# Performance work log

Hardware: AMD Instinct MI355X
Metric: run time of the kernel (lower is better)

The kernel has to match this reference:

```python
import jax, jax.numpy as jnp
import numpy as np

N_LAYERS = 2
D_MODEL = 1024
D_INNER = 2 * D_MODEL
D_STATE = 16
D_CONV = 4
DT_RANK = D_MODEL // 16  # 64
B_SZ, L = 1, 2048
EPS = 1e-5


def layernorm(x, w, b):
    mu = jnp.mean(x, axis=-1, keepdims=True)
    var = jnp.mean(jnp.square(x - mu), axis=-1, keepdims=True)
    return (x - mu) * jax.lax.rsqrt(var + EPS) * w + b


def mamba(x, in_w, cw, cb, xp_w, dtp_w, dtp_b, A_log, Dp, out_w):
    # x: [B, L, D_MODEL]
    Bn, Ln, _ = x.shape
    xz = jnp.einsum('bld,ed->ble', x, in_w)          # [B,L,2*D_INNER]
    xc, z = jnp.split(xz, 2, axis=-1)
    # causal depthwise conv1d (kernel D_CONV)
    xp = jnp.pad(xc, ((0, 0), (D_CONV - 1, 0), (0, 0)))
    xc = sum(xp[:, k:k + Ln, :] * cw[:, k] for k in range(D_CONV)) + cb
    xc = jax.nn.silu(xc)
    dbl = jnp.einsum('ble,re->blr', xc, xp_w)        # [B,L,DT_RANK+2*D_STATE]
    dt, Bm, Cm = jnp.split(dbl, [DT_RANK, DT_RANK + D_STATE], axis=-1)
    dt = jax.nn.softplus(jnp.einsum('blr,er->ble', dt, dtp_w) + dtp_b)  # [B,L,E]
    A = -jnp.exp(A_log)                              # [E,N], strictly negative
    dA = jnp.exp(dt[..., None] * A)                  # [B,L,E,N]
    dBu = (dt * xc)[..., None] * Bm[:, :, None, :]   # [B,L,E,N]

    def step(h, inp):
        dA_t, dBu_t, C_t = inp
        h = dA_t * h + dBu_t                         # [B,E,N]
        y = jnp.einsum('ben,bn->be', h, C_t)
        return h, y

    h0 = jnp.zeros((Bn, D_INNER, D_STATE), dA.dtype)
    _, ys = jax.lax.scan(step, h0, (dA.transpose(1, 0, 2, 3),
                                    dBu.transpose(1, 0, 2, 3),
                                    Cm.transpose(1, 0, 2)))
    y = ys.transpose(1, 0, 2) + xc * Dp              # [B,L,E]
    y = y * jax.nn.silu(z)
    return jnp.einsum('ble,de->bld', y, out_w)       # [B,L,D_MODEL]


def setup_inputs() -> dict:
    key = jax.random.key(0)
    ks = jax.random.split(key, 12)
    s = 0.02
    dt_init = np.log(np.expm1(0.01)).astype(np.float32)  # softplus^-1(0.01)
    A_row = jnp.log(jnp.arange(1, D_STATE + 1, dtype=jnp.float32))
    return {
        'x': jax.random.normal(ks[0], (B_SZ, L, D_MODEL), jnp.float32),
        'ln_w': jnp.ones((N_LAYERS, D_MODEL), jnp.float32),
        'ln_b': jnp.zeros((N_LAYERS, D_MODEL), jnp.float32),
        'in_proj_w': jax.random.normal(ks[1], (N_LAYERS, 2 * D_INNER, D_MODEL)) * s,
        'conv_w': jax.random.normal(ks[2], (N_LAYERS, D_INNER, D_CONV)) * 0.2,
        'conv_b': jnp.zeros((N_LAYERS, D_INNER), jnp.float32),
        'x_proj_w': jax.random.normal(ks[3], (N_LAYERS, DT_RANK + 2 * D_STATE, D_INNER)) * s,
        'dt_proj_w': jax.random.normal(ks[4], (N_LAYERS, D_INNER, DT_RANK)) * (DT_RANK ** -0.5),
        'dt_proj_b': jnp.full((N_LAYERS, D_INNER), dt_init),
        'A_log': jnp.broadcast_to(A_row, (N_LAYERS, D_INNER, D_STATE)).copy(),
        'D_skip': jnp.ones((N_LAYERS, D_INNER), jnp.float32),
        'out_proj_w': jax.random.normal(ks[5], (N_LAYERS, D_MODEL, D_INNER)) * s,
        'norm_f_w': jnp.ones((D_MODEL,), jnp.float32),
        'norm_f_b': jnp.zeros((D_MODEL,), jnp.float32),
    }


def reference(x, ln_w, ln_b, in_proj_w, conv_w, conv_b, x_proj_w, dt_proj_w,
              dt_proj_b, A_log, D_skip, out_proj_w, norm_f_w, norm_f_b):
    for i in range(N_LAYERS):
        h = layernorm(x, ln_w[i], ln_b[i])
        h = mamba(h, in_proj_w[i], conv_w[i], conv_b[i], x_proj_w[i],
                  dt_proj_w[i], dt_proj_b[i], A_log[i], D_skip[i], out_proj_w[i])
        x = h + x  # residual (dropout/drop_path are identity in eval)
    return layernorm(x, norm_f_w, norm_f_b)
```

## Files before the change

kernel.cpp:

```cpp
#include <hip/hip_runtime.h>
#include <hip/hip_bf16.h>
#include <math.h>

#define LSEQ 2048
#define DMODEL 1024
#define DINNER 2048
#define DSTATE 16
#define DCONV 4
#define DTRANK 64
#define RPROJ 96

#define CHUNK 16
#define NCHUNK (LSEQ / CHUNK)

#define XSPLIT 4

typedef __attribute__((ext_vector_type(8))) short bf16x8;
typedef __attribute__((ext_vector_type(4))) float f32x4;

__device__ __forceinline__ float softplusf(float x) {
    return (x > 20.f) ? x : log1pf(__expf(x));
}
__device__ __forceinline__ float siluf(float x) {
    return x / (1.f + __expf(-x));
}
__device__ __forceinline__ short f2bf(float f) {
    union { float f; unsigned u; } v; v.f = f;
    unsigned r = v.u + 0x7FFFu + ((v.u >> 16) & 1u);
    return (short)(r >> 16);
}
__device__ __forceinline__ float bf2f(short h) {
    union { unsigned u; float f; } v;
    v.u = ((unsigned)(unsigned short)h) << 16;
    return v.f;
}

__device__ __forceinline__ void cvt8(const float* __restrict__ s,
                                     short* __restrict__ d, int i) {
    const float4 a = *(const float4*)(s + i);
    const float4 b = *(const float4*)(s + i + 4);
    alignas(16) short h[8];
    h[0] = f2bf(a.x); h[1] = f2bf(a.y); h[2] = f2bf(a.z); h[3] = f2bf(a.w);
    h[4] = f2bf(b.x); h[5] = f2bf(b.y); h[6] = f2bf(b.z); h[7] = f2bf(b.w);
    *(uint4*)(d + i) = *(const uint4*)h;
}

__global__ __launch_bounds__(256) void cvt_weights(
    const float* __restrict__ s0, short* __restrict__ d0, int n0,
    const float* __restrict__ s1, short* __restrict__ d1, int n1,
    const float* __restrict__ s2, short* __restrict__ d2, int n2,
    const float* __restrict__ s3, short* __restrict__ d3, int n3)
{
    int i = (blockIdx.x * 256 + threadIdx.x) * 8;
    if (i < n0) { cvt8(s0, d0, i); return; }
    i -= n0;
    if (i < n1) { cvt8(s1, d1, i); return; }
    i -= n1;
    if (i < n2) { cvt8(s2, d2, i); return; }
    i -= n2;
    if (i < n3) { cvt8(s3, d3, i); return; }
}

__global__ __launch_bounds__(256) void ln_kernel(
    const float* __restrict__ x, const float* __restrict__ w,
    const float* __restrict__ b, float* __restrict__ outf,
    short* __restrict__ outb)
{
    __shared__ float s1[256], s2[256];
    const int row = blockIdx.x;
    const int tid = threadIdx.x;
    const float* xr = x + (size_t)row * DMODEL;
    float v[4];
    float s = 0.f, sq = 0.f;
#pragma unroll
    for (int k = 0; k < 4; k++) {
        v[k] = xr[k * 256 + tid];
        s += v[k];
        sq += v[k] * v[k];
    }
    s1[tid] = s; s2[tid] = sq;
    __syncthreads();
    for (int off = 128; off > 0; off >>= 1) {
        if (tid < off) { s1[tid] += s1[tid + off]; s2[tid] += s2[tid + off]; }
        __syncthreads();
    }
    const float mu = s1[0] * (1.f / DMODEL);
    const float var = s2[0] * (1.f / DMODEL) - mu * mu;
    const float rstd = rsqrtf(var + 1e-5f);
#pragma unroll
    for (int k = 0; k < 4; k++) {
        const int i = k * 256 + tid;
        const float o = (v[k] - mu) * rstd * w[i] + b[i];
        if (outf) outf[(size_t)row * DMODEL + i] = o;
        if (outb) outb[(size_t)row * DMODEL + i] = f2bf(o);
    }
}

template<int NJ, int MODE>
__global__ __launch_bounds__(256) void gemm_mfma(
    const short* __restrict__ A, int lda,
    const short* __restrict__ W, int ldw,
    float* __restrict__ Cf, short* __restrict__ Cb, int ldc,
    int M, int N, int K,
    const float* __restrict__ bias,
    const float* __restrict__ resid,
    size_t csplit)
{
    constexpr int BN = 32 * NJ;
    constexpr int HN = 16 * NJ;
    constexpr int WISS = BN / 64;
    __shared__ alignas(16) short As[64 * 32];
    __shared__ alignas(16) short Ws[BN * 32];

    const int tid = threadIdx.x;
    const int lane = tid & 63;
    const int w = tid >> 6;
    const int wr = w >> 1, wc = w & 1;
    const int row0 = blockIdx.y * 64;
    const int col0 = blockIdx.x * BN;
    const int kbeg = blockIdx.z * K;

    const int srow = tid >> 2;
    const int skch = ((tid & 3) ^ ((srow >> 1) & 3)) * 8;

    f32x4 acc[2][NJ];
#pragma unroll
    for (int i = 0; i < 2; i++)
#pragma unroll
        for (int j = 0; j < NJ; j++) acc[i][j] = (f32x4)0.f;

    const int lrow = lane & 15;
    const int q = lane >> 4;

    for (int kt = kbeg; kt < kbeg + K; kt += 32) {
        __syncthreads();
        {
            const short* gp = A + (size_t)(row0 + srow) * lda + kt + skch;
            __builtin_amdgcn_global_load_lds(
                (const __attribute__((address_space(1))) void*)gp,
                (__attribute__((address_space(3))) void*)(As + tid * 8), 16, 0, 0);
        }
#pragma unroll
        for (int j = 0; j < WISS; j++) {
            const int wrow = col0 + j * 64 + srow;
            if (wrow < N) {
                const short* gp = W + (size_t)wrow * ldw + kt + skch;
                __builtin_amdgcn_global_load_lds(
                    (const __attribute__((address_space(1))) void*)gp,
                    (__attribute__((address_space(3))) void*)(Ws + j * 2048 + tid * 8),
                    16, 0, 0);
            }
        }
        __syncthreads();

        bf16x8 af[2], bfr[NJ];
#pragma unroll
        for (int i = 0; i < 2; i++) {
            const int R = wr * 32 + i * 16 + lrow;
            af[i] = *(const bf16x8*)&As[R * 32 + ((q ^ ((R >> 1) & 3)) * 8)];
        }
#pragma unroll
        for (int j = 0; j < NJ; j++) {
            const int R = wc * HN + j * 16 + lrow;
            bfr[j] = *(const bf16x8*)&Ws[R * 32 + ((q ^ ((R >> 1) & 3)) * 8)];
        }
#pragma unroll
        for (int i = 0; i < 2; i++)
#pragma unroll
            for (int j = 0; j < NJ; j++)
                acc[i][j] = __builtin_amdgcn_mfma_f32_16x16x32_bf16(
                    af[i], bfr[j], acc[i][j], 0, 0, 0);
    }

    if (MODE == 0 && csplit) Cf += blockIdx.z * csplit;

    const int rbase = row0 + wr * 32;
    const int cbase = col0 + wc * HN;
#pragma unroll
    for (int i = 0; i < 2; i++) {
#pragma unroll
        for (int j = 0; j < NJ; j++) {
            const int gcol = cbase + j * 16 + lrow;
            if (gcol < N) {
#pragma unroll
                for (int r = 0; r < 4; r++) {
                    const int grow = rbase + i * 16 + (lane >> 4) * 4 + r;
                    float v = acc[i][j][r];
                    if (MODE == 2) v += resid[(size_t)grow * ldc + gcol];
                    if (MODE == 5) v = softplusf(v + bias[gcol]);
                    if (MODE == 3 || MODE == 5) {
                        Cb[(size_t)grow * ldc + gcol] = f2bf(v);
                    } else {
                        Cf[(size_t)grow * ldc + gcol] = v;
                    }
                }
            }
        }
    }
}

__global__ __launch_bounds__(256) void combine_xproj(
    const float* __restrict__ part,
    float* __restrict__ dbl, short* __restrict__ dblb)
{
    const int i = (blockIdx.x * 256 + threadIdx.x) * 4;
    const int S = LSEQ * RPROJ;
    float4 v = *(const float4*)(part + i);
#pragma unroll
    for (int s = 1; s < XSPLIT; s++) {
        const float4 p = *(const float4*)(part + s * S + i);
        v.x += p.x; v.y += p.y; v.z += p.z; v.w += p.w;
    }
    *(float4*)(dbl + i) = v;
    alignas(8) short h[4] = {f2bf(v.x), f2bf(v.y), f2bf(v.z), f2bf(v.w)};
    *(unsigned long long*)(dblb + i) = *(const unsigned long long*)h;
}

__global__ __launch_bounds__(256) void conv_silu_kernel(
    const short* __restrict__ xzb, const float* __restrict__ cw,
    const float* __restrict__ cb, short* __restrict__ xcb)
{
    const int g = blockIdx.x * 256 + threadIdx.x;
    const int t = g >> 8;
    const int c0 = (g & 255) * 8;
    float acc[8];
#pragma unroll
    for (int j = 0; j < 8; j++) acc[j] = cb[c0 + j];
#pragma unroll
    for (int k = 0; k < DCONV; k++) {
        const int tt = t - (DCONV - 1) + k;
        if (tt >= 0) {
            const bf16x8 v = *(const bf16x8*)(xzb + (size_t)tt * (2 * DINNER) + c0);
#pragma unroll
            for (int j = 0; j < 8; j++)
                acc[j] += bf2f(v[j]) * cw[(c0 + j) * DCONV + k];
        }
    }
    alignas(16) short h[8];
#pragma unroll
    for (int j = 0; j < 8; j++) h[j] = f2bf(siluf(acc[j]));
    *(uint4*)(xcb + (size_t)t * DINNER + c0) = *(const uint4*)h;
}

__global__ __launch_bounds__(256) void scan_pass1(
    const short* __restrict__ dtb,
    const short* __restrict__ xcb,
    const float* __restrict__ dbl,
    const float* __restrict__ A_log,
    float* __restrict__ S,
    float* __restrict__ sumdt)
{
    const int e = blockIdx.x * 256 + threadIdx.x;
    const int c = blockIdx.y;
    float a[DSTATE];
#pragma unroll
    for (int n = 0; n < DSTATE; n++) a[n] = -__expf(A_log[(size_t)e * DSTATE + n]);
    float h[DSTATE];
#pragma unroll
    for (int n = 0; n < DSTATE; n++) h[n] = 0.f;
    float sd = 0.f;

    __shared__ float sBC[CHUNK][32];
    for (int i = threadIdx.x; i < CHUNK * 32; i += 256) {
        const int tl = i >> 5, j = i & 31;
        sBC[tl][j] = dbl[(size_t)(c * CHUNK + tl) * RPROJ + DTRANK + j];
    }
    __syncthreads();

    const size_t rb = (size_t)c * CHUNK * DINNER + e;
    short dt_c = dtb[rb], xc_c = xcb[rb];
#pragma unroll
    for (int tl = 0; tl < CHUNK; tl++) {
        short dt_n = 0, xc_n = 0;
        if (tl + 1 < CHUNK) {
            dt_n = dtb[rb + (size_t)(tl + 1) * DINNER];
            xc_n = xcb[rb + (size_t)(tl + 1) * DINNER];
        }
        const float dtv = bf2f(dt_c);
        const float du = dtv * bf2f(xc_c);
        sd += dtv;
#pragma unroll
        for (int n = 0; n < DSTATE; n++) {
            const float dA = __expf(dtv * a[n]);
            h[n] = dA * h[n] + du * sBC[tl][n];
        }
        dt_c = dt_n; xc_c = xc_n;
    }
    sumdt[(size_t)c * DINNER + e] = sd;
#pragma unroll
    for (int n = 0; n < DSTATE; n++)
        S[((size_t)c * DSTATE + n) * DINNER + e] = h[n];
}

__global__ __launch_bounds__(256) void scan_pass2(
    const float* __restrict__ A_log,
    const float* __restrict__ sumdt,
    float* __restrict__ S)
{
    const int idx = blockIdx.x * 256 + threadIdx.x;
    const int e = idx & (DINNER - 1);
    const int n = idx >> 11;
    const float a = -__expf(A_log[(size_t)e * DSTATE + n]);
    float H = 0.f;
    for (int c = 0; c < NCHUNK; c++) {
        const size_t off = ((size_t)c * DSTATE + n) * DINNER + e;
        const float tmp = S[off];
        S[off] = H;
        const float P = __expf(a * sumdt[(size_t)c * DINNER + e]);
        H = P * H + tmp;
    }
}

__global__ __launch_bounds__(256) void scan_pass3(
    const short* __restrict__ dtb,
    const short* __restrict__ xcb,
    const float* __restrict__ dbl,
    const short* __restrict__ xzb,
    const float* __restrict__ A_log,
    const float* __restrict__ Dp,
    const float* __restrict__ S,
    short* __restrict__ yb)
{
    const int e = blockIdx.x * 256 + threadIdx.x;
    const int c = blockIdx.y;
    float a[DSTATE];
#pragma unroll
    for (int n = 0; n < DSTATE; n++) a[n] = -__expf(A_log[(size_t)e * DSTATE + n]);
    float h[DSTATE];
#pragma unroll
    for (int n = 0; n < DSTATE; n++)
        h[n] = S[((size_t)c * DSTATE + n) * DINNER + e];
    const float dskip = Dp[e];

    __shared__ float sBC[CHUNK][32];
    for (int i = threadIdx.x; i < CHUNK * 32; i += 256) {
        const int tl = i >> 5, j = i & 31;
        sBC[tl][j] = dbl[(size_t)(c * CHUNK + tl) * RPROJ + DTRANK + j];
    }
    __syncthreads();

    const size_t rb = (size_t)c * CHUNK * DINNER + e;
    const size_t zb = (size_t)c * CHUNK * (2 * DINNER) + DINNER + e;
    short dt_c = dtb[rb], xc_c = xcb[rb], z_c = xzb[zb];
#pragma unroll
    for (int tl = 0; tl < CHUNK; tl++) {
        short dt_n = 0, xc_n = 0, z_n = 0;
        if (tl + 1 < CHUNK) {
            dt_n = dtb[rb + (size_t)(tl + 1) * DINNER];
            xc_n = xcb[rb + (size_t)(tl + 1) * DINNER];
            z_n = xzb[zb + (size_t)(tl + 1) * (2 * DINNER)];
        }
        const float dtv = bf2f(dt_c);
        const float xcv = bf2f(xc_c);
        const float du = dtv * xcv;
        float yv = 0.f;
#pragma unroll
        for (int n = 0; n < DSTATE; n++) {
            const float dA = __expf(dtv * a[n]);
            h[n] = dA * h[n] + du * sBC[tl][n];
            yv += h[n] * sBC[tl][16 + n];
        }
        yv = (yv + xcv * dskip) * siluf(bf2f(z_c));
        yb[rb + (size_t)tl * DINNER] = f2bf(yv);
        dt_c = dt_n; xc_c = xc_n; z_c = z_n;
    }
}

extern "C" void kernel_launch(void* const* d_in, const int* in_sizes, int n_in,
                              void* d_out, int out_size, void* d_ws, size_t ws_size,
                              hipStream_t stream) {
    const float* x_in   = (const float*)d_in[0];
    const float* ln_w   = (const float*)d_in[1];
    const float* ln_b   = (const float*)d_in[2];
    const float* in_w   = (const float*)d_in[3];
    const float* conv_w = (const float*)d_in[4];
    const float* conv_b = (const float*)d_in[5];
    const float* xp_w   = (const float*)d_in[6];
    const float* dtp_w  = (const float*)d_in[7];
    const float* dtp_b  = (const float*)d_in[8];
    const float* A_log  = (const float*)d_in[9];
    const float* D_skip = (const float*)d_in[10];
    const float* out_w  = (const float*)d_in[11];
    const float* nf_w   = (const float*)d_in[12];
    const float* nf_b   = (const float*)d_in[13];
    float* out = (float*)d_out;

    float* w = (float*)d_ws;
    float* buf_x = w; w += (size_t)LSEQ * DMODEL;
    float* dbl   = w; w += (size_t)LSEQ * RPROJ;
    float* xpart = w; w += (size_t)XSPLIT * LSEQ * RPROJ;
    float* Sbuf  = w; w += (size_t)NCHUNK * DSTATE * DINNER;
    float* sumdt = w; w += (size_t)NCHUNK * DINNER;
    short* h_bf    = (short*)w; w += (size_t)LSEQ * DMODEL / 2;
    short* xz_bf   = (short*)w; w += (size_t)LSEQ * 2 * DINNER / 2;
    short* xc_bf   = (short*)w; w += (size_t)LSEQ * DINNER / 2;
    short* dt_bf   = (short*)w; w += (size_t)LSEQ * DINNER / 2;
    short* y_bf    = (short*)w; w += (size_t)LSEQ * DINNER / 2;
    short* dbl_bf  = (short*)w; w += (size_t)LSEQ * RPROJ / 2 + 1;
    short* in_w_bf  = (short*)w; w += (size_t)2 * (2 * DINNER) * DMODEL / 2;
    short* xp_w_bf  = (short*)w; w += (size_t)2 * RPROJ * DINNER / 2;
    short* dtp_w_bf = (short*)w; w += (size_t)2 * DINNER * DTRANK / 2;
    short* out_w_bf = (short*)w; w += (size_t)2 * DMODEL * DINNER / 2;

    {
        const int n1 = 2 * (2 * DINNER) * DMODEL;
        const int n2 = 2 * RPROJ * DINNER;
        const int n3 = 2 * DMODEL * DINNER;
        const int n4 = 2 * DINNER * DTRANK;
        const int total = n1 + n2 + n3 + n4;
        cvt_weights<<<dim3(total / (256 * 8)), dim3(256), 0, stream>>>(
            in_w, in_w_bf, n1, xp_w, xp_w_bf, n2,
            out_w, out_w_bf, n3, dtp_w, dtp_w_bf, n4);
    }

    for (int layer = 0; layer < 2; layer++) {
        const float* resid_src = (layer == 0) ? x_in : buf_x;
        ln_kernel<<<dim3(LSEQ), dim3(256), 0, stream>>>(
            resid_src, ln_w + layer * DMODEL, ln_b + layer * DMODEL,
            nullptr, h_bf);
        gemm_mfma<4, 3><<<dim3((2 * DINNER) / 128, LSEQ / 64), dim3(256), 0, stream>>>(
            h_bf, DMODEL, in_w_bf + (size_t)layer * 2 * DINNER * DMODEL, DMODEL,
            nullptr, xz_bf, 2 * DINNER, LSEQ, 2 * DINNER, DMODEL, nullptr, nullptr, 0);
        conv_silu_kernel<<<dim3((LSEQ * DINNER / 8) / 256), dim3(256), 0, stream>>>(
            xz_bf, conv_w + (size_t)layer * DINNER * DCONV, conv_b + layer * DINNER,
            xc_bf);
        gemm_mfma<2, 0><<<dim3(2, LSEQ / 64, XSPLIT), dim3(256), 0, stream>>>(
            xc_bf, DINNER, xp_w_bf + (size_t)layer * RPROJ * DINNER, DINNER,
            xpart, nullptr, RPROJ, LSEQ, RPROJ, DINNER / XSPLIT, nullptr, nullptr,
            (size_t)LSEQ * RPROJ);
        combine_xproj<<<dim3((LSEQ * RPROJ / 4) / 256), dim3(256), 0, stream>>>(
            xpart, dbl, dbl_bf);
        gemm_mfma<4, 5><<<dim3(DINNER / 128, LSEQ / 64), dim3(256), 0, stream>>>(
            dbl_bf, RPROJ, dtp_w_bf + (size_t)layer * DINNER * DTRANK, DTRANK,
            nullptr, dt_bf, DINNER, LSEQ, DINNER, DTRANK,
            dtp_b + layer * DINNER, nullptr, 0);
        const float* Al = A_log + (size_t)layer * DINNER * DSTATE;
        scan_pass1<<<dim3(DINNER / 256, NCHUNK), dim3(256), 0, stream>>>(
            dt_bf, xc_bf, dbl, Al, Sbuf, sumdt);
        scan_pass2<<<dim3((DINNER * DSTATE) / 256), dim3(256), 0, stream>>>(
            Al, sumdt, Sbuf);
        scan_pass3<<<dim3(DINNER / 256, NCHUNK), dim3(256), 0, stream>>>(
            dt_bf, xc_bf, dbl, xz_bf, Al, D_skip + layer * DINNER, Sbuf, y_bf);
        gemm_mfma<2, 2><<<dim3(DMODEL / 64, LSEQ / 64), dim3(256), 0, stream>>>(
            y_bf, DINNER, out_w_bf + (size_t)layer * DMODEL * DINNER, DINNER,
            buf_x, nullptr, DMODEL, LSEQ, DMODEL, DINNER, nullptr, resid_src, 0);
    }
    ln_kernel<<<dim3(LSEQ), dim3(256), 0, stream>>>(buf_x, nf_w, nf_b, out, nullptr);
}
```

Baseline: 491.1 us.

## Double-buffer GEMM LDS tiles and prefetch loads in scan pass2

The MFMA GEMM now uses two LDS buffers. The next K-tile is issued with global_load_lds while the current tile is being multiplied, and the loop needs one barrier per iteration instead of two. The kernel is templated on MI for M-tile size, but every launch keeps MI=2, so tiles are unchanged. scan_pass2 software-prefetches the next chunk's state and sumdt to hide load latency in its serial loop. Double buffering doubles LDS use per block and may lower occupancy. It also relies on the global_load_lds writes being visible after a single barrier, with no explicit vmcnt wait.

Result: no change. 496.8 us (+1.2%).

```diff
diff --git a/kernel.cpp b/kernel.cpp
--- a/kernel.cpp
+++ b/kernel.cpp
@@ -96,7 +96,7 @@
     }
 }
 
-template<int NJ, int MODE>
+template<int MI, int NJ, int MODE>
 __global__ __launch_bounds__(256) void gemm_mfma(
     const short* __restrict__ A, int lda,
     const short* __restrict__ W, int ldw,
@@ -106,39 +106,42 @@
     const float* __restrict__ resid,
     size_t csplit)
 {
+    constexpr int BM = 32 * MI;
     constexpr int BN = 32 * NJ;
-    constexpr int HN = 16 * NJ;
+    constexpr int AISS = BM / 64;
     constexpr int WISS = BN / 64;
-    __shared__ alignas(16) short As[64 * 32];
-    __shared__ alignas(16) short Ws[BN * 32];
+    __shared__ alignas(16) short As[2][BM * 32];
+    __shared__ alignas(16) short Ws[2][BN * 32];
 
     const int tid = threadIdx.x;
     const int lane = tid & 63;
     const int w = tid >> 6;
     const int wr = w >> 1, wc = w & 1;
-    const int row0 = blockIdx.y * 64;
+    const int row0 = blockIdx.y * BM;
     const int col0 = blockIdx.x * BN;
     const int kbeg = blockIdx.z * K;
 
     const int srow = tid >> 2;
     const int skch = ((tid & 3) ^ ((srow >> 1) & 3)) * 8;
 
-    f32x4 acc[2][NJ];
-#pragma unroll
-    for (int i = 0; i < 2; i++)
+    f32x4 acc[MI][NJ];
+#pragma unroll
+    for (int i = 0; i < MI; i++)
 #pragma unroll
         for (int j = 0; j < NJ; j++) acc[i][j] = (f32x4)0.f;
 
     const int lrow = lane & 15;
     const int q = lane >> 4;
-
-    for (int kt = kbeg; kt < kbeg + K; kt += 32) {
-        __syncthreads();
-        {
-            const short* gp = A + (size_t)(row0 + srow) * lda + kt + skch;
+    const int NIT = K / 32;
+
+    auto stage = [&](int p, int kt) {
+#pragma unroll
+        for (int j = 0; j < AISS; j++) {
+            const short* gp = A + (size_t)(row0 + j * 64 + srow) * lda + kt + skch;
             __builtin_amdgcn_global_load_lds(
                 (const __attribute__((address_space(1))) void*)gp,
-                (__attribute__((address_space(3))) void*)(As + tid * 8), 16, 0, 0);
+                (__attribute__((address_space(3))) void*)(&As[p][j * 2048 + tid * 8]),
+                16, 0, 0);
         }
 #pragma unroll
         for (int j = 0; j < WISS; j++) {
@@ -147,37 +150,44 @@
                 const short* gp = W + (size_t)wrow * ldw + kt + skch;
                 __builtin_amdgcn_global_load_lds(
                     (const __attribute__((address_space(1))) void*)gp,
-                    (__attribute__((address_space(3))) void*)(Ws + j * 2048 + tid * 8),
+                    (__attribute__((address_space(3))) void*)(&Ws[p][j * 2048 + tid * 8]),
                     16, 0, 0);
             }
         }
-        __syncthreads();
-
-        bf16x8 af[2], bfr[NJ];
-#pragma unroll
-        for (int i = 0; i < 2; i++) {
-            const int R = wr * 32 + i * 16 + lrow;
-            af[i] = *(const bf16x8*)&As[R * 32 + ((q ^ ((R >> 1) & 3)) * 8)];
+    };
+
+    stage(0, kbeg);
+    __syncthreads();
+    for (int it = 0; it < NIT; ++it) {
+        const int p = it & 1;
+        if (it + 1 < NIT) stage(p ^ 1, kbeg + (it + 1) * 32);
+
+        bf16x8 af[MI], bfr[NJ];
+#pragma unroll
+        for (int i = 0; i < MI; i++) {
+            const int R = wr * (16 * MI) + i * 16 + lrow;
+            af[i] = *(const bf16x8*)&As[p][R * 32 + ((q ^ ((R >> 1) & 3)) * 8)];
         }
 #pragma unroll
         for (int j = 0; j < NJ; j++) {
-            const int R = wc * HN + j * 16 + lrow;
-            bfr[j] = *(const bf16x8*)&Ws[R * 32 + ((q ^ ((R >> 1) & 3)) * 8)];
-        }
-#pragma unroll
-        for (int i = 0; i < 2; i++)
+            const int R = wc * (16 * NJ) + j * 16 + lrow;
+            bfr[j] = *(const bf16x8*)&Ws[p][R * 32 + ((q ^ ((R >> 1) & 3)) * 8)];
+        }
+#pragma unroll
+        for (int i = 0; i < MI; i++)
 #pragma unroll
             for (int j = 0; j < NJ; j++)
                 acc[i][j] = __builtin_amdgcn_mfma_f32_16x16x32_bf16(
                     af[i], bfr[j], acc[i][j], 0, 0, 0);
+        __syncthreads();
     }
 
     if (MODE == 0 && csplit) Cf += blockIdx.z * csplit;
 
-    const int rbase = row0 + wr * 32;
-    const int cbase = col0 + wc * HN;
-#pragma unroll
-    for (int i = 0; i < 2; i++) {
+    const int rbase = row0 + wr * (16 * MI);
+    const int cbase = col0 + wc * (16 * NJ);
+#pragma unroll
+    for (int i = 0; i < MI; i++) {
 #pragma unroll
         for (int j = 0; j < NJ; j++) {
             const int gcol = cbase + j * 16 + lrow;
@@ -301,13 +311,20 @@
     const int e = idx & (DINNER - 1);
     const int n = idx >> 11;
     const float a = -__expf(A_log[(size_t)e * DSTATE + n]);
+    const size_t base = (size_t)n * DINNER + e;
+    const size_t cstr = (size_t)DSTATE * DINNER;
     float H = 0.f;
+    float sc = S[base];
+    float sd = sumdt[e];
     for (int c = 0; c < NCHUNK; c++) {
-        const size_t off = ((size_t)c * DSTATE + n) * DINNER + e;
-        const float tmp = S[off];
-        S[off] = H;
-        const float P = __expf(a * sumdt[(size_t)c * DINNER + e]);
-        H = P * H + tmp;
+        float sc_n = 0.f, sd_n = 0.f;
+        if (c + 1 < NCHUNK) {
+            sc_n = S[base + (size_t)(c + 1) * cstr];
+            sd_n = sumdt[(size_t)(c + 1) * DINNER + e];
+        }
+        S[base + (size_t)c * cstr] = H;
+        H = __expf(a * sd) * H + sc;
+        sc = sc_n; sd = sd_n;
     }
 }
 
@@ -418,19 +435,19 @@
         ln_kernel<<<dim3(LSEQ), dim3(256), 0, stream>>>(
             resid_src, ln_w + layer * DMODEL, ln_b + layer * DMODEL,
             nullptr, h_bf);
-        gemm_mfma<4, 3><<<dim3((2 * DINNER) / 128, LSEQ / 64), dim3(256), 0, stream>>>(
+        gemm_mfma<2, 4, 3><<<dim3((2 * DINNER) / 128, LSEQ / 64), dim3(256), 0, stream>>>(
             h_bf, DMODEL, in_w_bf + (size_t)layer * 2 * DINNER * DMODEL, DMODEL,
             nullptr, xz_bf, 2 * DINNER, LSEQ, 2 * DINNER, DMODEL, nullptr, nullptr, 0);
         conv_silu_kernel<<<dim3((LSEQ * DINNER / 8) / 256), dim3(256), 0, stream>>>(
             xz_bf, conv_w + (size_t)layer * DINNER * DCONV, conv_b + layer * DINNER,
             xc_bf);
-        gemm_mfma<2, 0><<<dim3(2, LSEQ / 64, XSPLIT), dim3(256), 0, stream>>>(
+        gemm_mfma<2, 2, 0><<<dim3(2, LSEQ / 64, XSPLIT), dim3(256), 0, stream>>>(
             xc_bf, DINNER, xp_w_bf + (size_t)layer * RPROJ * DINNER, DINNER,
             xpart, nullptr, RPROJ, LSEQ, RPROJ, DINNER / XSPLIT, nullptr, nullptr,
             (size_t)LSEQ * RPROJ);
         combine_xproj<<<dim3((LSEQ * RPROJ / 4) / 256), dim3(256), 0, stream>>>(
             xpart, dbl, dbl_bf);
-        gemm_mfma<4, 5><<<dim3(DINNER / 128, LSEQ / 64), dim3(256), 0, stream>>>(
+        gemm_mfma<2, 4, 5><<<dim3(DINNER / 128, LSEQ / 64), dim3(256), 0, stream>>>(
             dbl_bf, RPROJ, dtp_w_bf + (size_t)layer * DINNER * DTRANK, DTRANK,
             nullptr, dt_bf, DINNER, LSEQ, DINNER, DTRANK,
             dtp_b + layer * DINNER, nullptr, 0);
@@ -441,7 +458,7 @@
             Al, sumdt, Sbuf);
         scan_pass3<<<dim3(DINNER / 256, NCHUNK), dim3(256), 0, stream>>>(
             dt_bf, xc_bf, dbl, xz_bf, Al, D_skip + layer * DINNER, Sbuf, y_bf);
-        gemm_mfma<2, 2><<<dim3(DMODEL / 64, LSEQ / 64), dim3(256), 0, stream>>>(
+        gemm_mfma<2, 2, 2><<<dim3(DMODEL / 64, LSEQ / 64), dim3(256), 0, stream>>>(
             y_bf, DINNER, out_w_bf + (size_t)layer * DMODEL * DINNER, DINNER,
             buf_x, nullptr, DMODEL, LSEQ, DMODEL, DINNER, nullptr, resid_src, 0);
     }
```
